# Performance work log

Hardware: AMD Instinct MI355X
Metric: run time of the kernel (lower is better)

## Reference

```python
import jax, jax.numpy as jnp
import numpy as np

N, T, A, H, I, E = 50000, 25, 16, 128, 64, 800000
LN_EPS = 1e-5


def setup_inputs() -> dict:
    key = jax.random.key(0)
    ks = jax.random.split(key, 24)
    s = 0.05
    d = {}
    d['actions'] = jax.random.normal(ks[0], (N, T, A), jnp.float32)
    d['hidden'] = jax.random.normal(ks[1], (1, N, H), jnp.float32)
    d['src'] = jax.random.randint(ks[2], (E,), 0, N, jnp.int32)
    d['dst'] = jax.random.randint(ks[3], (E,), 0, N, jnp.int32)
    # GRU (torch layout: W_ih (3H, A), W_hh (3H, H), gates r,z,n)
    d['W_ih'] = jax.random.normal(ks[4], (3 * H, A), jnp.float32) * s
    d['W_hh'] = jax.random.normal(ks[5], (3 * H, H), jnp.float32) * s
    d['b_ih'] = jnp.zeros((3 * H,), jnp.float32)
    d['b_hh'] = jnp.zeros((3 * H,), jnp.float32)
    # LayerNorm feature_norm
    d['ln_g'] = jnp.ones((H,), jnp.float32)
    d['ln_b'] = jnp.zeros((H,), jnp.float32)
    # GraphConv (DGL norm='both'): weight (in, out), bias (out,)
    d['Wg'] = jax.random.normal(ks[6], (H, H), jnp.float32) * s
    d['bg'] = jnp.full((H,), 0.1, jnp.float32)
    # Four Gaussian heads (torch Linear: W (out, in))
    for i, name in enumerate(['zia_mu', 'zia_std', 'zig_mu', 'zig_std']):
        d['W_' + name] = jax.random.normal(ks[7 + i], (I, H), jnp.float32) * s
        d['b_' + name] = jnp.full((I,), 0.1, jnp.float32)
    return d


def _gru(x_tnf, h0, W_ih, W_hh, b_ih, b_hh):
    # x_tnf: (T, N, A); h0: (N, H). Precompute input projections for all steps.
    gi_all = jnp.einsum('tna,ga->tng', x_tnf, W_ih) + b_ih  # (T, N, 3H)

    def step(h, gi):
        gh = h @ W_hh.T + b_hh
        i_r, i_z, i_n = jnp.split(gi, 3, axis=-1)
        h_r, h_z, h_n = jnp.split(gh, 3, axis=-1)
        r = jax.nn.sigmoid(i_r + h_r)
        z = jax.nn.sigmoid(i_z + h_z)
        n = jnp.tanh(i_n + r * h_n)
        h_new = (1.0 - z) * n + z * h
        return h_new, None

    h_final, _ = jax.lax.scan(step, h0, gi_all)
    return h_final  # (N, H)


def _graph_conv(src, dst, x, Wg, bg):
    ones = jnp.ones((src.shape[0],), x.dtype)
    deg_out = jax.ops.segment_sum(ones, src, num_segments=N)
    deg_in = jax.ops.segment_sum(ones, dst, num_segments=N)
    norm_src = jnp.where(deg_out > 0, deg_out, 1.0) ** -0.5
    norm_dst = jnp.where(deg_in > 0, deg_in, 1.0) ** -0.5
    m = (x * norm_src[:, None])[src]                 # gather (E, H)
    agg = jax.ops.segment_sum(m, dst, num_segments=N)  # scatter-add (N, H)
    return (agg * norm_dst[:, None]) @ Wg + bg


def _layernorm(x, g, b):
    mu = jnp.mean(x, axis=-1, keepdims=True)
    var = jnp.var(x, axis=-1, keepdims=True)
    return (x - mu) * jax.lax.rsqrt(var + LN_EPS) * g + b


def reference(actions, hidden, src, dst, W_ih, W_hh, b_ih, b_hh, ln_g, ln_b,
              Wg, bg, W_zia_mu, b_zia_mu, W_zia_std, b_zia_std,
              W_zig_mu, b_zig_mu, W_zig_std, b_zig_std):
    x_tnf = jnp.transpose(actions, (1, 0, 2))  # actions.transpose(1,0)
    h = _gru(x_tnf, hidden[0], W_ih, W_hh, b_ih, b_hh)  # temp_rnn_state.squeeze(0)
    x = _layernorm(h, ln_g, ln_b)
    x = _graph_conv(src, dst, x, Wg, bg)
    zIA_mu = x @ W_zia_mu.T + b_zia_mu
    zIA_std = jax.nn.softplus(x @ W_zia_std.T + b_zia_std)
    zIG_mu = x @ W_zig_mu.T + b_zig_mu
    zIG_std = jax.nn.softplus(x @ W_zig_std.T + b_zig_std)
    # Normal(mu, std) params for both dists + rnn state
    return zIG_mu, zIG_std, zIA_mu, zIA_std, h
```

## Files before the change

### kernel.cpp

```cpp
#include <hip/hip_runtime.h>
#include <hip/hip_bf16.h>
#include <math.h>

constexpr int N_NODES = 50000;
constexpr int T_STEPS = 25;
constexpr int A_DIM   = 16;
constexpr int H_DIM   = 128;
constexpr int G3      = 3 * H_DIM;
constexpr int E_EDGES = 800000;
constexpr int I_DIM   = 64;
constexpr float LN_EPS = 1e-5f;
constexpr int NT = (N_NODES + 31) / 32;
constexpr int NT16 = N_NODES / 16;
constexpr int SXS = 408;
constexpr int SHS = 136;

using bf16x8 = __attribute__((ext_vector_type(8))) short;
using f32x4  = __attribute__((ext_vector_type(4))) float;

static __device__ __forceinline__ float fast_rcp(float x) { return __builtin_amdgcn_rcpf(x); }
static __device__ __forceinline__ float sigm(float x) { return fast_rcp(1.f + __expf(-x)); }
static __device__ __forceinline__ float tanh_fast(float x) {
    return fmaf(2.f, fast_rcp(1.f + __expf(-2.f * x)), -1.f);
}
static __device__ __forceinline__ float softplus_f(float x) {
    return (x > 20.f) ? x : __logf(1.f + __expf(x));
}
static __device__ __forceinline__ unsigned short f2bf(float f) {
    __hip_bfloat16 b = __float2bfloat16(f);
    return *(unsigned short*)&b;
}


__global__ void k_zero(int* deg_out, int* deg_in, int* cursor, int* esrc) {
    for (int i = blockIdx.x * blockDim.x + threadIdx.x; i < E_EDGES; i += gridDim.x * blockDim.x) {
        esrc[i] = 0;
        if (i < N_NODES) { deg_out[i] = 0; deg_in[i] = 0; cursor[i] = 0; }
    }
}

__global__ void k_hist(const int* __restrict__ src, const int* __restrict__ dst,
                       int* __restrict__ deg_out, int* __restrict__ deg_in) {
    for (int e = blockIdx.x * blockDim.x + threadIdx.x; e < E_EDGES; e += gridDim.x * blockDim.x) {
        int s = src[e], d = dst[e];
        if (s >= 0 && s < N_NODES) atomicAdd(&deg_out[s], 1);
        if (d >= 0 && d < N_NODES) atomicAdd(&deg_in[d], 1);
    }
}

__launch_bounds__(1024)
__global__ void k_scan(const int* __restrict__ deg, int* __restrict__ offs) {
    __shared__ int wsum[16];
    __shared__ int carry;
    const int tid = threadIdx.x;
    const int lane = tid & 63, wid = tid >> 6;
    if (tid == 0) carry = 0;
    __syncthreads();
    for (int base = 0; base < N_NODES; base += 1024) {
        int i = base + tid;
        int v = (i < N_NODES) ? deg[i] : 0;
        int x = v;
        #pragma unroll
        for (int off = 1; off < 64; off <<= 1) {
            int yv = __shfl_up(x, off);
            if (lane >= off) x += yv;
        }
        if (lane == 63) wsum[wid] = x;
        __syncthreads();
        if (wid == 0 && lane < 16) {
            int s = wsum[lane];
            #pragma unroll
            for (int off = 1; off < 16; off <<= 1) {
                int yv = __shfl_up(s, off, 16);
                if (lane >= off) s += yv;
            }
            wsum[lane] = s;
        }
        __syncthreads();
        int excl = carry + (wid > 0 ? wsum[wid - 1] : 0) + x - v;
        if (i < N_NODES) offs[i] = excl;
        __syncthreads();
        if (tid == 0) carry += wsum[15];
        __syncthreads();
    }
    if (tid == 0) offs[N_NODES] = carry;
}

__global__ void k_scatter(const int* __restrict__ src, const int* __restrict__ dst,
                          const int* __restrict__ offs, int* __restrict__ cursor,
                          int* __restrict__ esrc) {
    for (int e = blockIdx.x * blockDim.x + threadIdx.x; e < E_EDGES; e += gridDim.x * blockDim.x) {
        int d = dst[e];
        if (d < 0 || d >= N_NODES) continue;
        int pos = offs[d] + atomicAdd(&cursor[d], 1);
        if (pos >= 0 && pos < E_EDGES) esrc[pos] = src[e];
    }
}

__launch_bounds__(512, 4)
__global__ void k_gru(const float* __restrict__ actions,
                      const float* __restrict__ hidden,
                      const float* __restrict__ W_ih,
                      const float* __restrict__ W_hh,
                      const float* __restrict__ b_ih,
                      const float* __restrict__ b_hh,
                      float* __restrict__ h_out) {
    __shared__ __align__(16) unsigned short sX[32 * SXS];
    __shared__ __align__(16) unsigned short sH[32 * SHS];

    const int tid  = threadIdx.x;
    const int w    = tid >> 6;
    const int lane = tid & 63;
    const int quad = lane >> 4;
    const int l16  = lane & 15;
    const int j    = 16 * w + l16;

    bf16x8 Bhh[3][4];
    #pragma unroll
    for (int gt = 0; gt < 3; ++gt) {
        const float* rowp = W_hh + (size_t)(gt * H_DIM + j) * H_DIM;
        #pragma unroll
        for (int kc = 0; kc < 4; ++kc) {
            const float* p = rowp + kc * 32 + quad * 8;
            float4 f0 = *(const float4*)p;
            float4 f1 = *(const float4*)(p + 4);
            bf16x8 v;
            v[0] = f2bf(f0.x); v[1] = f2bf(f0.y); v[2] = f2bf(f0.z); v[3] = f2bf(f0.w);
            v[4] = f2bf(f1.x); v[5] = f2bf(f1.y); v[6] = f2bf(f1.z); v[7] = f2bf(f1.w);
            Bhh[gt][kc] = v;
        }
    }
    bf16x8 Bih[3];
    #pragma unroll
    for (int gt = 0; gt < 3; ++gt) {
        bf16x8 v;
        #pragma unroll
        for (int q = 0; q < 8; ++q) v[q] = 0;
        if (quad < 2) {
            const float* p = W_ih + (size_t)(gt * H_DIM + j) * A_DIM + quad * 8;
            float4 f0 = *(const float4*)p;
            float4 f1 = *(const float4*)(p + 4);
            v[0] = f2bf(f0.x); v[1] = f2bf(f0.y); v[2] = f2bf(f0.z); v[3] = f2bf(f0.w);
            v[4] = f2bf(f1.x); v[5] = f2bf(f1.y); v[6] = f2bf(f1.z); v[7] = f2bf(f1.w);
        }
        Bih[gt] = v;
    }
    const float br   = b_ih[j] + b_hh[j];
    const float bz   = b_ih[H_DIM + j] + b_hh[H_DIM + j];
    const float bn_i = b_ih[2 * H_DIM + j];
    const float bn_h = b_hh[2 * H_DIM + j];
    const f32x4 cr0 = {br, br, br, br};
    const f32x4 cz0 = {bz, bz, bz, bz};
    const f32x4 cn0 = {bn_i, bn_i, bn_i, bn_i};
    const f32x4 ch0 = {bn_h, bn_h, bn_h, bn_h};

    for (int tile = blockIdx.x; tile < NT; tile += gridDim.x) {
        const int base = tile * 32;
        for (int idx = tid; idx < 32 * SXS; idx += 512) {
            int nl = idx / SXS, p = idx - nl * SXS;
            int n = base + nl;
            float f = (p < 400 && n < N_NODES) ? actions[(size_t)n * 400 + p] : 0.f;
            sX[nl * SXS + p] = f2bf(f);
        }
        for (int idx = tid; idx < 32 * H_DIM; idx += 512) {
            int nl = idx >> 7, k = idx & 127;
            int n = base + nl;
            sH[nl * SHS + k] = f2bf((n < N_NODES) ? hidden[(size_t)n * H_DIM + k] : 0.f);
        }
        float hp[2][4];
        #pragma unroll
        for (int m = 0; m < 2; ++m)
            #pragma unroll
            for (int r = 0; r < 4; ++r) {
                int n = base + m * 16 + quad * 4 + r;
                hp[m][r] = (n < N_NODES) ? hidden[(size_t)n * H_DIM + j] : 0.f;
            }
        __syncthreads();

        for (int t = 0; t < T_STEPS; ++t) {
            #pragma unroll
            for (int m = 0; m < 2; ++m) {
                bf16x8 ax = *(const bf16x8*)&sX[(m * 16 + l16) * SXS + t * 16 + quad * 8];
                if (quad >= 2) {
                    #pragma unroll
                    for (int q = 0; q < 8; ++q) ax[q] = 0;
                }
                f32x4 Cr = __builtin_amdgcn_mfma_f32_16x16x32_bf16(ax, Bih[0], cr0, 0, 0, 0);
                f32x4 Cz = __builtin_amdgcn_mfma_f32_16x16x32_bf16(ax, Bih[1], cz0, 0, 0, 0);
                f32x4 Cn = __builtin_amdgcn_mfma_f32_16x16x32_bf16(ax, Bih[2], cn0, 0, 0, 0);
                f32x4 Ch = ch0;
                #pragma unroll
                for (int kc = 0; kc < 4; ++kc) {
                    bf16x8 ah = *(const bf16x8*)&sH[(m * 16 + l16) * SHS + kc * 32 + quad * 8];
                    Cr = __builtin_amdgcn_mfma_f32_16x16x32_bf16(ah, Bhh[0][kc], Cr, 0, 0, 0);
                    Cz = __builtin_amdgcn_mfma_f32_16x16x32_bf16(ah, Bhh[1][kc], Cz, 0, 0, 0);
                    Ch = __builtin_amdgcn_mfma_f32_16x16x32_bf16(ah, Bhh[2][kc], Ch, 0, 0, 0);
                }
                #pragma unroll
                for (int r = 0; r < 4; ++r) {
                    float rg = sigm(Cr[r]);
                    float zg = sigm(Cz[r]);
                    float ng = tanh_fast(Cn[r] + rg * Ch[r]);
                    hp[m][r] = ng + zg * (hp[m][r] - ng);
                }
            }
            if (t < T_STEPS - 1) {
                __syncthreads();
                #pragma unroll
                for (int m = 0; m < 2; ++m)
                    #pragma unroll
                    for (int r = 0; r < 4; ++r)
                        sH[(m * 16 + quad * 4 + r) * SHS + j] = f2bf(hp[m][r]);
                __syncthreads();
            }
        }
        #pragma unroll
        for (int m = 0; m < 2; ++m)
            #pragma unroll
            for (int r = 0; r < 4; ++r) {
                int n = base + m * 16 + quad * 4 + r;
                if (n < N_NODES) h_out[(size_t)n * H_DIM + j] = hp[m][r];
            }
        __syncthreads();
    }
}

__global__ void k_stats(const float* __restrict__ h, const int* __restrict__ deg_out,
                        float4* __restrict__ pqr) {
    int n = blockIdx.x * (blockDim.x >> 6) + (threadIdx.x >> 6);
    int lane = threadIdx.x & 63;
    if (n >= N_NODES) return;
    float v0 = h[(size_t)n * H_DIM + lane];
    float v1 = h[(size_t)n * H_DIM + 64 + lane];
    float s = v0 + v1, qq = v0 * v0 + v1 * v1;
    #pragma unroll
    for (int m = 32; m; m >>= 1) { s += __shfl_xor(s, m); qq += __shfl_xor(qq, m); }
    float mu = s * (1.f / H_DIM);
    float var = fmaxf(qq * (1.f / H_DIM) - mu * mu, 0.f);
    float inv = rsqrtf(var + LN_EPS);
    int d = deg_out[n];
    float ns = rsqrtf((float)(d > 0 ? d : 1));
    if (lane == 0) pqr[n] = make_float4(inv * ns, mu * inv * ns, ns, 0.f);
}

__global__ void k_comb(const float* __restrict__ Wg, const float* __restrict__ bg,
                       const float* __restrict__ Wig_mu, const float* __restrict__ big_mu,
                       const float* __restrict__ Wig_std, const float* __restrict__ big_std,
                       const float* __restrict__ Wia_mu, const float* __restrict__ bia_mu,
                       const float* __restrict__ Wia_std, const float* __restrict__ bia_std,
                       unsigned short* __restrict__ Wcomb, float* __restrict__ bcomb) {
    const int r = blockIdx.x;
    const int t = threadIdx.x;
    const int rr = r & 63;
    const float* Wh; const float* bh;
    switch (r >> 6) {
        case 0:  Wh = Wig_mu;  bh = big_mu;  break;
        case 1:  Wh = Wig_std; bh = big_std; break;
        case 2:  Wh = Wia_mu;  bh = bia_mu;  break;
        default: Wh = Wia_std; bh = bia_std; break;
    }
    __shared__ float sWr[H_DIM];
    sWr[t] = Wh[(size_t)rr * H_DIM + t];
    __syncthreads();
    const float4* wrow = (const float4*)(Wg + (size_t)t * H_DIM);
    float acc = 0.f;
    #pragma unroll 8
    for (int c4 = 0; c4 < 32; ++c4) {
        float4 v = wrow[c4];
        acc = fmaf(v.x, sWr[4 * c4    ], acc);
        acc = fmaf(v.y, sWr[4 * c4 + 1], acc);
        acc = fmaf(v.z, sWr[4 * c4 + 2], acc);
        acc = fmaf(v.w, sWr[4 * c4 + 3], acc);
    }
    Wcomb[r * H_DIM + t] = f2bf(acc);
    if (t == 0) {
        float s = bh[rr];
        for (int c = 0; c < H_DIM; ++c) s = fmaf(bg[c], sWr[c], s);
        bcomb[r] = s;
    }
}

__launch_bounds__(256)
__global__ void k_fused(const float* __restrict__ h,
                        const int* __restrict__ offs, const int* __restrict__ esrc,
                        const float4* __restrict__ pqr,
                        const float* __restrict__ ln_g, const float* __restrict__ ln_b,
                        const unsigned short* __restrict__ Wcomb,
                        const float* __restrict__ bcomb,
                        float* __restrict__ out) {
    __shared__ __align__(16) unsigned short yl[16][136];

    const int tid  = threadIdx.x;
    const int w    = tid >> 6;
    const int lane = tid & 63;
    const int l16  = lane & 15;
    const int quad = lane >> 4;
    const long long NI = (long long)N_NODES * I_DIM;

    bf16x8 B[4][4];
    float bc[4];
    #pragma unroll
    for (int ct = 0; ct < 4; ++ct) {
        int col = (w * 4 + ct) * 16 + l16;
        bc[ct] = bcomb[col];
        #pragma unroll
        for (int kc = 0; kc < 4; ++kc)
            B[ct][kc] = *(const bf16x8*)&Wcomb[col * H_DIM + kc * 32 + quad * 8];
    }
    const float2 g2 = *(const float2*)&ln_g[2 * lane];
    const float2 b2 = *(const float2*)&ln_b[2 * lane];

    for (int tile = blockIdx.x; tile < NT16; tile += gridDim.x) {
        const int base = tile * 16;
        #pragma unroll
        for (int i = 0; i < 4; ++i) {
            const int nl = w * 4 + i;
            const int n  = base + nl;
            const int s0 = offs[n], s1 = offs[n + 1];
            float ax = 0.f, ay = 0.f, sq = 0.f, sr = 0.f;
            for (int e0 = s0; e0 < s1; e0 += 64) {
                int sv = (e0 + lane < s1) ? esrc[e0 + lane] : 0;
                const int cnt = min(64, s1 - e0);
                for (int k = 0; k < cnt; ++k) {
                    int s = __shfl(sv, k);
                    float4 P = pqr[s];
                    float2 hv = *(const float2*)&h[(size_t)s * H_DIM + 2 * lane];
                    ax = fmaf(P.x, hv.x, ax);
                    ay = fmaf(P.x, hv.y, ay);
                    sq += P.y; sr += P.z;
                }
            }
            const int d = s1 - s0;
            const float nd = rsqrtf((float)(d > 0 ? d : 1));
            float y0 = (g2.x * (ax - sq) + b2.x * sr) * nd;
            float y1 = (g2.y * (ay - sq) + b2.y * sr) * nd;
            unsigned int pk = ((unsigned int)f2bf(y1) << 16) | (unsigned int)f2bf(y0);
            *(unsigned int*)&yl[nl][2 * lane] = pk;
        }
        __syncthreads();
        bf16x8 A[4];
        #pragma unroll
        for (int kc = 0; kc < 4; ++kc)
            A[kc] = *(const bf16x8*)&yl[l16][kc * 32 + quad * 8];
        #pragma unroll
        for (int ct = 0; ct < 4; ++ct) {
            f32x4 C = {0.f, 0.f, 0.f, 0.f};
            #pragma unroll
            for (int kc = 0; kc < 4; ++kc)
                C = __builtin_amdgcn_mfma_f32_16x16x32_bf16(A[kc], B[ct][kc], C, 0, 0, 0);
            const int col  = (w * 4 + ct) * 16 + l16;
            const int head = col >> 6;
            const int wi   = col & 63;
            const bool sp  = (col & 64) != 0;
            #pragma unroll
            for (int r_ = 0; r_ < 4; ++r_) {
                const int node = base + quad * 4 + r_;
                float v = C[r_] + bc[ct];
                if (sp) v = softplus_f(v);
                out[(long long)head * NI + (long long)node * I_DIM + wi] = v;
            }
        }
        __syncthreads();
    }
}

extern "C" void kernel_launch(void* const* d_in, const int* in_sizes, int n_in,
                              void* d_out, int out_size, void* d_ws, size_t ws_size,
                              hipStream_t stream) {
    const float* actions = (const float*)d_in[0];
    const float* hidden  = (const float*)d_in[1];
    const int*   src     = (const int*)d_in[2];
    const int*   dst     = (const int*)d_in[3];
    const float* W_ih    = (const float*)d_in[4];
    const float* W_hh    = (const float*)d_in[5];
    const float* b_ih    = (const float*)d_in[6];
    const float* b_hh    = (const float*)d_in[7];
    const float* ln_g    = (const float*)d_in[8];
    const float* ln_b    = (const float*)d_in[9];
    const float* Wg      = (const float*)d_in[10];
    const float* bg      = (const float*)d_in[11];
    const float* Wia_mu  = (const float*)d_in[12];
    const float* bia_mu  = (const float*)d_in[13];
    const float* Wia_std = (const float*)d_in[14];
    const float* bia_std = (const float*)d_in[15];
    const float* Wig_mu  = (const float*)d_in[16];
    const float* big_mu  = (const float*)d_in[17];
    const float* Wig_std = (const float*)d_in[18];
    const float* big_std = (const float*)d_in[19];
    float* out = (float*)d_out;

    char* w = (char*)d_ws;
    const size_t SZN = 200064;
    int*   deg_out = (int*)(w);
    int*   deg_in  = (int*)(w + SZN);
    int*   offs    = (int*)(w + 2 * SZN);
    int*   cursor  = (int*)(w + 2 * SZN + 200128);
    int*   esrc    = (int*)(w + 3 * SZN + 200128);
    float4* pqrA   = (float4*)(w + 3 * SZN + 200128 + 3200000);
    unsigned short* Wcomb = (unsigned short*)(w + 3 * SZN + 200128 + 3200000 + 800000);
    float* bcomb   = (float*)(w + 3 * SZN + 200128 + 3200000 + 800000 + 65536);

    k_zero<<<2048, 256, 0, stream>>>(deg_out, deg_in, cursor, esrc);
    k_hist<<<1024, 256, 0, stream>>>(src, dst, deg_out, deg_in);
    k_scan<<<1, 1024, 0, stream>>>(deg_in, offs);
    k_scatter<<<1024, 256, 0, stream>>>(src, dst, offs, cursor, esrc);
    k_comb<<<256, 128, 0, stream>>>(Wg, bg, Wig_mu, big_mu, Wig_std, big_std,
                                    Wia_mu, bia_mu, Wia_std, bia_std, Wcomb, bcomb);

    float* h_f = out + (size_t)4 * N_NODES * I_DIM;
    k_gru<<<NT, 512, 0, stream>>>(actions, hidden, W_ih, W_hh, b_ih, b_hh, h_f);

    k_stats<<<(N_NODES + 3) / 4, 256, 0, stream>>>(h_f, deg_out, pqrA);

    k_fused<<<2048, 256, 0, stream>>>(h_f, offs, esrc, pqrA, ln_g, ln_b,
                                      Wcomb, bcomb, out);
}
```

Before: 753.6 us.

## Fuse LayerNorm and src-norm into GRU epilogue, gather bf16 rows, parallel scan

The GRU epilogue now stages the final hidden tile in shared memory, writes h with coalesced float4 stores, and computes LayerNorm plus the source-degree normalisation per node. It stores the result as packed bf16 rows (zA), so the aggregation kernel gathers half-size pre-normalised rows and skips the separate stats kernel and the per-edge pqr lookups. The single-block serial prefix scan is replaced by a three-kernel block-parallel scan, and the fused kernel's grid is set to one block per tile. This path depends on the workspace being large enough, and it adds bf16 rounding before aggregation instead of after.

```diff
diff --git a/kernel.cpp b/kernel.cpp
--- a/kernel.cpp
+++ b/kernel.cpp
@@ -14,6 +14,7 @@
 constexpr int NT16 = N_NODES / 16;
 constexpr int SXS = 408;
 constexpr int SHS = 136;
+constexpr int SCB = 196;
 
 using bf16x8 = __attribute__((ext_vector_type(8))) short;
 using f32x4  = __attribute__((ext_vector_type(4))) float;
@@ -29,6 +30,11 @@
 static __device__ __forceinline__ unsigned short f2bf(float f) {
     __hip_bfloat16 b = __float2bfloat16(f);
     return *(unsigned short*)&b;
+}
+static __device__ __forceinline__ float2 bfp(unsigned int u) {
+    union { unsigned int i; float f; } lo, hi;
+    lo.i = u << 16; hi.i = u & 0xFFFF0000u;
+    return make_float2(lo.f, hi.f);
 }
 
 
@@ -48,42 +54,50 @@
     }
 }
 
-__launch_bounds__(1024)
-__global__ void k_scan(const int* __restrict__ deg, int* __restrict__ offs) {
-    __shared__ int wsum[16];
-    __shared__ int carry;
-    const int tid = threadIdx.x;
-    const int lane = tid & 63, wid = tid >> 6;
-    if (tid == 0) carry = 0;
+__global__ void k_scan1(const int* __restrict__ deg, int* __restrict__ offs,
+                        int* __restrict__ bsum) {
+    __shared__ int wsum[4];
+    const int tid = threadIdx.x, lane = tid & 63, wid = tid >> 6;
+    const int i = blockIdx.x * 256 + tid;
+    int v = (i < N_NODES) ? deg[i] : 0;
+    int x = v;
+    #pragma unroll
+    for (int off = 1; off < 64; off <<= 1) {
+        int yv = __shfl_up(x, off);
+        if (lane >= off) x += yv;
+    }
+    if (lane == 63) wsum[wid] = x;
     __syncthreads();
-    for (int base = 0; base < N_NODES; base += 1024) {
-        int i = base + tid;
-        int v = (i < N_NODES) ? deg[i] : 0;
-        int x = v;
-        #pragma unroll
-        for (int off = 1; off < 64; off <<= 1) {
-            int yv = __shfl_up(x, off);
-            if (lane >= off) x += yv;
-        }
-        if (lane == 63) wsum[wid] = x;
-        __syncthreads();
-        if (wid == 0 && lane < 16) {
-            int s = wsum[lane];
-            #pragma unroll
-            for (int off = 1; off < 16; off <<= 1) {
-                int yv = __shfl_up(s, off, 16);
-                if (lane >= off) s += yv;
-            }
-            wsum[lane] = s;
-        }
-        __syncthreads();
-        int excl = carry + (wid > 0 ? wsum[wid - 1] : 0) + x - v;
-        if (i < N_NODES) offs[i] = excl;
-        __syncthreads();
-        if (tid == 0) carry += wsum[15];
-        __syncthreads();
-    }
-    if (tid == 0) offs[N_NODES] = carry;
+    int pre = 0;
+    #pragma unroll
+    for (int w2 = 0; w2 < 3; ++w2) if (w2 < wid) pre += wsum[w2];
+    if (i < N_NODES) offs[i] = pre + x - v;
+    if (tid == 255) bsum[blockIdx.x] = pre + x;
+}
+
+__global__ void k_scan2(const int* __restrict__ bsum, int* __restrict__ boffs,
+                        int* __restrict__ offs) {
+    __shared__ int wsum[4];
+    const int tid = threadIdx.x, lane = tid & 63, wid = tid >> 6;
+    int v = (tid < SCB) ? bsum[tid] : 0;
+    int x = v;
+    #pragma unroll
+    for (int off = 1; off < 64; off <<= 1) {
+        int yv = __shfl_up(x, off);
+        if (lane >= off) x += yv;
+    }
+    if (lane == 63) wsum[wid] = x;
+    __syncthreads();
+    int pre = 0;
+    #pragma unroll
+    for (int w2 = 0; w2 < 3; ++w2) if (w2 < wid) pre += wsum[w2];
+    if (tid < SCB) boffs[tid] = pre + x - v;
+    if (tid == 255) offs[N_NODES] = pre + x;
+}
+
+__global__ void k_scan3(const int* __restrict__ boffs, int* __restrict__ offs) {
+    const int i = blockIdx.x * 256 + threadIdx.x;
+    if (i < N_NODES) offs[i] += boffs[blockIdx.x];
 }
 
 __global__ void k_scatter(const int* __restrict__ src, const int* __restrict__ dst,
@@ -104,6 +118,10 @@
                       const float* __restrict__ W_hh,
                       const float* __restrict__ b_ih,
                       const float* __restrict__ b_hh,
+                      const float* __restrict__ ln_g,
+                      const float* __restrict__ ln_b,
+                      const int* __restrict__ deg_out,
+                      unsigned int* __restrict__ zA,
                       float* __restrict__ h_out) {
     __shared__ __align__(16) unsigned short sX[32 * SXS];
     __shared__ __align__(16) unsigned short sH[32 * SHS];
@@ -153,6 +171,8 @@
     const f32x4 cz0 = {bz, bz, bz, bz};
     const f32x4 cn0 = {bn_i, bn_i, bn_i, bn_i};
     const f32x4 ch0 = {bn_h, bn_h, bn_h, bn_h};
+    const float2 lg2 = *(const float2*)&ln_g[2 * lane];
+    const float2 lb2 = *(const float2*)&ln_b[2 * lane];
 
     for (int tile = blockIdx.x; tile < NT; tile += gridDim.x) {
         const int base = tile * 32;
@@ -214,13 +234,49 @@
                 __syncthreads();
             }
         }
+
+        __syncthreads();
+        float* sF = (float*)sX;
         #pragma unroll
         for (int m = 0; m < 2; ++m)
             #pragma unroll
-            for (int r = 0; r < 4; ++r) {
-                int n = base + m * 16 + quad * 4 + r;
-                if (n < N_NODES) h_out[(size_t)n * H_DIM + j] = hp[m][r];
-            }
+            for (int r = 0; r < 4; ++r)
+                sF[(m * 16 + quad * 4 + r) * 128 + j] = hp[m][r];
+        __syncthreads();
+        #pragma unroll
+        for (int it = 0; it < 2; ++it) {
+            int idx4 = tid + it * 512;
+            int n = base + (idx4 >> 5);
+            if (idx4 < 1024 && n < N_NODES)
+                *(float4*)&h_out[(size_t)base * 128 + (size_t)idx4 * 4] =
+                    *(const float4*)&sF[idx4 * 4];
+        }
+        if (zA) {
+            #pragma unroll
+            for (int i = 0; i < 4; ++i) {
+                const int nl = w * 4 + i;
+                const int n = base + nl;
+                if (n < N_NODES) {
+                    float v0 = sF[nl * 128 + 2 * lane];
+                    float v1 = sF[nl * 128 + 2 * lane + 1];
+                    float s = v0 + v1, qq = v0 * v0 + v1 * v1;
+                    #pragma unroll
+                    for (int mm = 32; mm; mm >>= 1) {
+                        s  += __shfl_xor(s, mm);
+                        qq += __shfl_xor(qq, mm);
+                    }
+                    float mu  = s * (1.f / H_DIM);
+                    float var = fmaxf(qq * (1.f / H_DIM) - mu * mu, 0.f);
+                    float inv = rsqrtf(var + LN_EPS);
+                    int dg = deg_out[n];
+                    float ns = rsqrtf((float)(dg > 0 ? dg : 1));
+                    float z0 = (lg2.x * (v0 - mu) * inv + lb2.x) * ns;
+                    float z1 = (lg2.y * (v1 - mu) * inv + lb2.y) * ns;
+                    zA[(size_t)n * 64 + lane] =
+                        ((unsigned int)f2bf(z1) << 16) | (unsigned int)f2bf(z0);
+                }
+            }
+        }
         __syncthreads();
     }
 }
@@ -280,8 +336,10 @@
     }
 }
 
+template<bool USEZ>
 __launch_bounds__(256)
 __global__ void k_fused(const float* __restrict__ h,
+                        const unsigned int* __restrict__ zA,
                         const int* __restrict__ offs, const int* __restrict__ esrc,
                         const float4* __restrict__ pqr,
                         const float* __restrict__ ln_g, const float* __restrict__ ln_b,
@@ -321,19 +379,51 @@
             for (int e0 = s0; e0 < s1; e0 += 64) {
                 int sv = (e0 + lane < s1) ? esrc[e0 + lane] : 0;
                 const int cnt = min(64, s1 - e0);
-                for (int k = 0; k < cnt; ++k) {
-                    int s = __shfl(sv, k);
-                    float4 P = pqr[s];
-                    float2 hv = *(const float2*)&h[(size_t)s * H_DIM + 2 * lane];
-                    ax = fmaf(P.x, hv.x, ax);
-                    ay = fmaf(P.x, hv.y, ay);
-                    sq += P.y; sr += P.z;
+                int k = 0;
+                if (USEZ) {
+                    for (; k + 4 <= cnt; k += 4) {
+                        int sa = __shfl(sv, k),     sb = __shfl(sv, k + 1);
+                        int sc = __shfl(sv, k + 2), sd = __shfl(sv, k + 3);
+                        unsigned int za = zA[(size_t)sa * 64 + lane];
+                        unsigned int zb = zA[(size_t)sb * 64 + lane];
+                        unsigned int zc = zA[(size_t)sc * 64 + lane];
+                        unsigned int zd = zA[(size_t)sd * 64 + lane];
+                        float2 fa = bfp(za), fb = bfp(zb), fc = bfp(zc), fd = bfp(zd);
+                        ax += (fa.x + fb.x) + (fc.x + fd.x);
+                        ay += (fa.y + fb.y) + (fc.y + fd.y);
+                    }
+                    for (; k < cnt; ++k) {
+                        int s = __shfl(sv, k);
+                        float2 f = bfp(zA[(size_t)s * 64 + lane]);
+                        ax += f.x; ay += f.y;
+                    }
+                } else {
+                    for (; k + 2 <= cnt; k += 2) {
+                        int sa = __shfl(sv, k), sb = __shfl(sv, k + 1);
+                        float4 Pa = pqr[sa], Pb = pqr[sb];
+                        float2 ha = *(const float2*)&h[(size_t)sa * H_DIM + 2 * lane];
+                        float2 hb = *(const float2*)&h[(size_t)sb * H_DIM + 2 * lane];
+                        ax = fmaf(Pa.x, ha.x, ax); ay = fmaf(Pa.x, ha.y, ay);
+                        ax = fmaf(Pb.x, hb.x, ax); ay = fmaf(Pb.x, hb.y, ay);
+                        sq += Pa.y + Pb.y; sr += Pa.z + Pb.z;
+                    }
+                    for (; k < cnt; ++k) {
+                        int s = __shfl(sv, k);
+                        float4 P = pqr[s];
+                        float2 hv = *(const float2*)&h[(size_t)s * H_DIM + 2 * lane];
+                        ax = fmaf(P.x, hv.x, ax); ay = fmaf(P.x, hv.y, ay);
+                        sq += P.y; sr += P.z;
+                    }
                 }
             }
             const int d = s1 - s0;
             const float nd = rsqrtf((float)(d > 0 ? d : 1));
-            float y0 = (g2.x * (ax - sq) + b2.x * sr) * nd;
-            float y1 = (g2.y * (ay - sq) + b2.y * sr) * nd;
+            float y0, y1;
+            if (USEZ) { y0 = ax * nd; y1 = ay * nd; }
+            else {
+                y0 = (g2.x * (ax - sq) + b2.x * sr) * nd;
+                y1 = (g2.y * (ay - sq) + b2.y * sr) * nd;
+            }
             unsigned int pk = ((unsigned int)f2bf(y1) << 16) | (unsigned int)f2bf(y0);
             *(unsigned int*)&yl[nl][2 * lane] = pk;
         }
@@ -396,22 +486,35 @@
     int*   offs    = (int*)(w + 2 * SZN);
     int*   cursor  = (int*)(w + 2 * SZN + 200128);
     int*   esrc    = (int*)(w + 3 * SZN + 200128);
-    float4* pqrA   = (float4*)(w + 3 * SZN + 200128 + 3200000);
-    unsigned short* Wcomb = (unsigned short*)(w + 3 * SZN + 200128 + 3200000 + 800000);
-    float* bcomb   = (float*)(w + 3 * SZN + 200128 + 3200000 + 800000 + 65536);
+    char*  p2      = w + 3 * SZN + 200128 + 3200000;
+    int*   bsum    = (int*)(p2);
+    int*   boffs   = (int*)(p2 + 1024);
+    unsigned short* Wcomb = (unsigned short*)(p2 + 2048);
+    float* bcomb   = (float*)(p2 + 2048 + 65536);
+    char*  p3      = p2 + 2048 + 65536 + 1024;
+    float4* pqrA   = (float4*)p3;
+    unsigned int* zA = (unsigned int*)p3;
+    const bool useZ = ws_size >= (size_t)(4068928 + 12800000);
 
     k_zero<<<2048, 256, 0, stream>>>(deg_out, deg_in, cursor, esrc);
     k_hist<<<1024, 256, 0, stream>>>(src, dst, deg_out, deg_in);
-    k_scan<<<1, 1024, 0, stream>>>(deg_in, offs);
+    k_scan1<<<SCB, 256, 0, stream>>>(deg_in, offs, bsum);
+    k_scan2<<<1, 256, 0, stream>>>(bsum, boffs, offs);
+    k_scan3<<<SCB, 256, 0, stream>>>(boffs, offs);
     k_scatter<<<1024, 256, 0, stream>>>(src, dst, offs, cursor, esrc);
     k_comb<<<256, 128, 0, stream>>>(Wg, bg, Wig_mu, big_mu, Wig_std, big_std,
                                     Wia_mu, bia_mu, Wia_std, bia_std, Wcomb, bcomb);
 
     float* h_f = out + (size_t)4 * N_NODES * I_DIM;
-    k_gru<<<NT, 512, 0, stream>>>(actions, hidden, W_ih, W_hh, b_ih, b_hh, h_f);
-
-    k_stats<<<(N_NODES + 3) / 4, 256, 0, stream>>>(h_f, deg_out, pqrA);
-
-    k_fused<<<2048, 256, 0, stream>>>(h_f, offs, esrc, pqrA, ln_g, ln_b,
-                                      Wcomb, bcomb, out);
-}
+    k_gru<<<NT, 512, 0, stream>>>(actions, hidden, W_ih, W_hh, b_ih, b_hh,
+                                  ln_g, ln_b, deg_out, useZ ? zA : nullptr, h_f);
+
+    if (useZ) {
+        k_fused<true><<<NT16, 256, 0, stream>>>(h_f, zA, offs, esrc, pqrA,
+                                                ln_g, ln_b, Wcomb, bcomb, out);
+    } else {
+        k_stats<<<(N_NODES + 3) / 4, 256, 0, stream>>>(h_f, deg_out, pqrA);
+        k_fused<false><<<NT16, 256, 0, stream>>>(h_f, zA, offs, esrc, pqrA,
+                                                 ln_g, ln_b, Wcomb, bcomb, out);
+    }
+}
```

Measured after the change: 637.4 us. 15.4% less time.
